# Optimization experiments

Measured on AMD Instinct MI355X. Metric: run time of the kernel, lower is better.

The kernel has to match this reference:

```python
import jax, jax.numpy as jnp
import numpy as np

N_NODES = 100000
N_EDGES = 1600000
N_GRAPHS = 1024
D_IN = 128
D_HID = 128
D_OUT = 2


def setup_inputs() -> dict:
    key = jax.random.key(0)
    ks = jax.random.split(key, 12)
    x = jax.random.normal(ks[0], (N_NODES, D_IN), dtype=jnp.float32)
    edge_index = jax.random.randint(ks[1], (2, N_EDGES), 0, N_NODES, dtype=jnp.int32)
    batch = jnp.sort(jax.random.randint(ks[2], (N_NODES,), 0, N_GRAPHS, dtype=jnp.int32))
    def lin(k, fan_in, fan_out):
        bound = 1.0 / np.sqrt(fan_in)
        kw, kb = jax.random.split(k)
        W = jax.random.uniform(kw, (fan_in, fan_out), minval=-bound, maxval=bound, dtype=jnp.float32)
        b = jax.random.uniform(kb, (fan_out,), minval=-bound, maxval=bound, dtype=jnp.float32)
        return W, b
    W1, b1 = lin(ks[3], D_IN, D_HID)
    W2, b2 = lin(ks[4], D_HID, D_HID)
    fc1_w, fc1_b = lin(ks[5], D_HID, D_HID)
    fc2_w, fc2_b = lin(ks[6], D_HID, D_OUT)
    return {"x": x, "edge_index": edge_index, "batch": batch,
            "W1": W1, "b1": b1, "W2": W2, "b2": b2,
            "fc1_w": fc1_w, "fc1_b": fc1_b, "fc2_w": fc2_w, "fc2_b": fc2_b}


def gcn_conv(x, W, b, src, dst, deg_inv_sqrt, n_nodes):
    # GCNConv: out = D^-1/2 (A + I) D^-1/2 (x W) + b, using edge list with self-loops
    h = x @ W  # [N, d_out]
    norm = deg_inv_sqrt[src] * deg_inv_sqrt[dst]  # [E+N]
    msg = h[src] * norm[:, None]  # gather + scale
    out = jnp.zeros((n_nodes, h.shape[1]), dtype=h.dtype).at[dst].add(msg)
    return out + b


def reference(x, edge_index, batch, W1, b1, W2, b2, fc1_w, fc1_b, fc2_w, fc2_b):
    n = x.shape[0]
    loops = jnp.arange(n, dtype=edge_index.dtype)
    src = jnp.concatenate([edge_index[0], loops])  # add self-loops (PyG default)
    dst = jnp.concatenate([edge_index[1], loops])
    deg = jnp.zeros((n,), dtype=x.dtype).at[dst].add(1.0)
    deg_inv_sqrt = jax.lax.rsqrt(deg)  # deg >= 1 due to self-loops

    h = jax.nn.relu(gcn_conv(x, W1, b1, src, dst, deg_inv_sqrt, n))
    # dropout p=0.5 is identity in eval mode
    h = jax.nn.relu(gcn_conv(h, W2, b2, src, dst, deg_inv_sqrt, n))

    # global_mean_pool over batch assignment
    sums = jax.ops.segment_sum(h, batch, num_segments=N_GRAPHS)
    cnts = jax.ops.segment_sum(jnp.ones((n,), dtype=h.dtype), batch, num_segments=N_GRAPHS)
    pooled = sums / jnp.maximum(cnts, 1.0)[:, None]  # [G, d]

    g = jax.nn.relu(pooled @ fc1_w + fc1_b)
    logits = g @ fc2_w + fc2_b
    return jax.nn.log_softmax(logits, axis=1)
```

## Files before the change

### kernel.cpp

```cpp
#include <hip/hip_runtime.h>
#include <hip/hip_fp16.h>
#include <math.h>


#define D_FEAT 128
#define BSHIFT 9
#define BNODES 512
#define CHUNK 4096
#define CAPB 16384

using half8   = __attribute__((ext_vector_type(8))) _Float16;
using half4   = __attribute__((ext_vector_type(4))) _Float16;
using floatx4 = __attribute__((ext_vector_type(4))) float;
using floatx2 = __attribute__((ext_vector_type(2))) float;

__global__ void __launch_bounds__(256) binA_kernel(const int* __restrict__ edges,
                                                   int* __restrict__ gcur,
                                                   int* __restrict__ binned, int E, int nb) {
    __shared__ int h[256];
    __shared__ int cur[256];
    __shared__ int base[256];
    int t = threadIdx.x;
    int c0 = blockIdx.x * CHUNK;
    int sv[CHUNK / 256], bv[CHUNK / 256];
    int i0 = c0 + t * (CHUNK / 256);
    if (i0 + (CHUNK / 256) <= E) {
#pragma unroll
        for (int k = 0; k < CHUNK / 256; k += 4) {
            int4 s4 = *(const int4*)&edges[i0 + k];
            int4 d4 = *(const int4*)&edges[E + i0 + k];
            bv[k + 0] = d4.x >> BSHIFT; sv[k + 0] = ((d4.x & (BNODES - 1)) << 17) | s4.x;
            bv[k + 1] = d4.y >> BSHIFT; sv[k + 1] = ((d4.y & (BNODES - 1)) << 17) | s4.y;
            bv[k + 2] = d4.z >> BSHIFT; sv[k + 2] = ((d4.z & (BNODES - 1)) << 17) | s4.z;
            bv[k + 3] = d4.w >> BSHIFT; sv[k + 3] = ((d4.w & (BNODES - 1)) << 17) | s4.w;
        }
    } else {
#pragma unroll
        for (int k = 0; k < CHUNK / 256; ++k) {
            int i = i0 + k;
            if (i < E) {
                int s = edges[i], d = edges[E + i];
                bv[k] = d >> BSHIFT;
                sv[k] = ((d & (BNODES - 1)) << 17) | s;
            } else bv[k] = -1;
        }
    }
    h[t] = 0;
    __syncthreads();
#pragma unroll
    for (int k = 0; k < CHUNK / 256; ++k)
        if (bv[k] >= 0) atomicAdd(&h[bv[k]], 1);
    __syncthreads();
    if (t < nb && h[t] > 0) base[t] = atomicAdd(&gcur[t], h[t]);
    cur[t] = 0;
    __syncthreads();
#pragma unroll
    for (int k = 0; k < CHUNK / 256; ++k)
        if (bv[k] >= 0) {
            int b = bv[k];
            int r = atomicAdd(&cur[b], 1);
            int pos = base[b] + r;
            if (pos < CAPB) binned[b * CAPB + pos] = sv[k];
        }
}

__global__ void __launch_bounds__(256) binB1_kernel(const int* __restrict__ binned,
                                                    const int* __restrict__ gcur,
                                                    float* __restrict__ dis,
                                                    int* __restrict__ rowptr,
                                                    int* __restrict__ gcursor,
                                                    int N, int E, int nb) {
    __shared__ int hist[BNODES];
    __shared__ int sdata[256];
    int t = threadIdx.x;
    int b = blockIdx.x;
    int node0 = b << BSHIFT;
    int cnt = gcur[b];
    int gval = (t < nb) ? gcur[t] : 0;
    sdata[t] = gval;
    __syncthreads();
    for (int d = 1; d < 256; d <<= 1) {
        int u = (t >= d) ? sdata[t - d] : 0;
        __syncthreads();
        sdata[t] += u;
        __syncthreads();
    }
    int e0 = sdata[b] - cnt;
    __syncthreads();
    const int* bin = binned + (size_t)b * CAPB;
    hist[t] = 0; hist[t + 256] = 0;
    __syncthreads();
    for (int i = t; i < cnt; i += 256) atomicAdd(&hist[bin[i] >> 17], 1);
    __syncthreads();
    int a0 = hist[2 * t], a1 = hist[2 * t + 1];
    int pair = a0 + a1;
    sdata[t] = pair;
    __syncthreads();
    for (int d = 1; d < 256; d <<= 1) {
        int u = (t >= d) ? sdata[t - d] : 0;
        __syncthreads();
        sdata[t] += u;
        __syncthreads();
    }
    int excl = sdata[t] - pair;
    int p0 = e0 + excl, p1 = e0 + excl + a0;
    gcursor[(b << BSHIFT) + 2 * t] = p0;
    gcursor[(b << BSHIFT) + 2 * t + 1] = p1;
    int n0 = node0 + 2 * t, n1 = node0 + 2 * t + 1;
    if (n0 < N) { rowptr[n0] = p0; dis[n0] = rsqrtf((float)a0 + 1.0f); }
    if (n1 < N) { rowptr[n1] = p1; dis[n1] = rsqrtf((float)a1 + 1.0f); }
    if (b == nb - 1 && t == 0) rowptr[N] = E;
}

__global__ void __launch_bounds__(256) binB2_kernel(const int* __restrict__ binned,
                                                    const int* __restrict__ gcur,
                                                    const int* __restrict__ gcursor,
                                                    int* __restrict__ csr, int nb) {
    __shared__ int cur[BNODES];
    int t = threadIdx.x;
    int b = blockIdx.x;
    int cnt = gcur[b];
    const int* bin = binned + (size_t)b * CAPB;
    cur[t] = gcursor[(b << BSHIFT) + t];
    cur[t + 256] = gcursor[(b << BSHIFT) + t + 256];
    __syncthreads();
    for (int i = t; i < cnt; i += 256) {
        int v = bin[i];
        int p = atomicAdd(&cur[v >> 17], 1);
        csr[p] = v & 0x1FFFF;
    }
}

__global__ void wprep_kernel(const float* __restrict__ W1, const float* __restrict__ W2,
                             _Float16* __restrict__ Wt1, _Float16* __restrict__ Wt2) {
    int i = blockIdx.x * blockDim.x + threadIdx.x;
    int n = i >> 7, k = i & 127;
    Wt1[i] = (_Float16)W1[k * 128 + n];
    Wt2[i] = (_Float16)W2[k * 128 + n];
}

template <bool HALF_IN>
__global__ void __launch_bounds__(256) gemm_mfma_kernel(const void* __restrict__ Xv,
                                                        const _Float16* __restrict__ WtG,
                                                        const float* __restrict__ dis,
                                                        unsigned char* __restrict__ Y8, int N) {
    __shared__ _Float16 wt[128][136];
    int t = threadIdx.x;
    int row0 = blockIdx.x * 64;

#pragma unroll
    for (int i = 0; i < 8; ++i) {
        int c = t + i * 256;
        int r = c >> 4, c8 = (c & 15) * 8;
        *(half8*)&wt[r][c8] = *(const half8*)&WtG[r * 128 + c8];
    }

    int wave = t >> 6, lane = t & 63;
    int m = lane & 15, quad = lane >> 4;
    int grow = row0 + wave * 16 + m;

    half8 a[4];
    if (grow < N) {
        if (HALF_IN) {
            const _Float16* Xp = (const _Float16*)Xv;
#pragma unroll
            for (int k = 0; k < 4; ++k)
                a[k] = *(const half8*)&Xp[(size_t)grow * 128 + k * 32 + quad * 8];
        } else {
            const float* Xp = (const float*)Xv;
#pragma unroll
            for (int k = 0; k < 4; ++k) {
                float4 v0 = *(const float4*)&Xp[(size_t)grow * 128 + k * 32 + quad * 8];
                float4 v1 = *(const float4*)&Xp[(size_t)grow * 128 + k * 32 + quad * 8 + 4];
                a[k] = (half8){(_Float16)v0.x, (_Float16)v0.y, (_Float16)v0.z, (_Float16)v0.w,
                               (_Float16)v1.x, (_Float16)v1.y, (_Float16)v1.z, (_Float16)v1.w};
            }
        }
    } else {
#pragma unroll
        for (int k = 0; k < 4; ++k) a[k] = (half8){};
    }
    __syncthreads();

    floatx4 acc[8];
#pragma unroll
    for (int nt = 0; nt < 8; ++nt) acc[nt] = (floatx4){0.f, 0.f, 0.f, 0.f};
#pragma unroll
    for (int nt = 0; nt < 8; ++nt) {
#pragma unroll
        for (int k = 0; k < 4; ++k) {
            half8 bfr = *(const half8*)&wt[nt * 16 + m][k * 32 + quad * 8];
            acc[nt] = __builtin_amdgcn_mfma_f32_16x16x32_f16(a[k], bfr, acc[nt], 0, 0, 0);
        }
    }
    int orow = row0 + wave * 16 + quad * 4;
#pragma unroll
    for (int r = 0; r < 4; ++r) {
        int row = orow + r;
        if (row < N) {
            float dr = dis[row];
#pragma unroll
            for (int nt = 0; nt < 8; ++nt) {
                float v = acc[nt][r] * dr;
                unsigned char q =
                    (unsigned char)(__builtin_amdgcn_cvt_pk_fp8_f32(v, v, 0, false) & 0xff);
                Y8[(size_t)row * 128 + nt * 16 + m] = q;
            }
        }
    }
}

__global__ void __launch_bounds__(256) agg_kernel(const unsigned char* __restrict__ H8,
                                                  const int* __restrict__ rowptr,
                                                  const int* __restrict__ csr,
                                                  const float* __restrict__ dis,
                                                  const float* __restrict__ bias,
                                                  _Float16* __restrict__ out, int N) {
    int v = (blockIdx.x * blockDim.x + threadIdx.x) >> 6;
    int lane = threadIdx.x & 63;
    if (v >= N) return;
    int half = lane >> 5, sl = lane & 31;
    int r0 = rowptr[v], r1 = rowptr[v + 1];
    float dv = dis[v];
    unsigned fo = (unsigned)(sl << 2);

    floatx2 a01, a23;
    {
        unsigned int u = *(const unsigned int*)(H8 + (((unsigned)v << 7) | fo));
        floatx2 lo = __builtin_amdgcn_cvt_pk_f32_fp8(u, false);
        floatx2 hi = __builtin_amdgcn_cvt_pk_f32_fp8(u, true);
        floatx2 hf = {0.5f, 0.5f};
        a01 = hf * lo;
        a23 = hf * hi;
    }
#define ACC(uu)                                                         \
        {                                                               \
            a01 += __builtin_amdgcn_cvt_pk_f32_fp8(uu, false);          \
            a23 += __builtin_amdgcn_cvt_pk_f32_fp8(uu, true);           \
        }
#define ACCW(uu, ww)                                                    \
        {                                                               \
            floatx2 w2 = {(ww), (ww)};                                  \
            a01 += w2 * __builtin_amdgcn_cvt_pk_f32_fp8(uu, false);     \
            a23 += w2 * __builtin_amdgcn_cvt_pk_f32_fp8(uu, true);      \
        }
    int e = r0 + half;
    for (; e + 14 < r1; e += 16) {
        int s0 = csr[e],      s1 = csr[e + 2],  s2 = csr[e + 4],  s3 = csr[e + 6];
        int s4 = csr[e + 8],  s5 = csr[e + 10], s6 = csr[e + 12], s7 = csr[e + 14];
        unsigned int u0 = *(const unsigned int*)(H8 + (((unsigned)s0 << 7) | fo));
        unsigned int u1 = *(const unsigned int*)(H8 + (((unsigned)s1 << 7) | fo));
        unsigned int u2 = *(const unsigned int*)(H8 + (((unsigned)s2 << 7) | fo));
        unsigned int u3 = *(const unsigned int*)(H8 + (((unsigned)s3 << 7) | fo));
        unsigned int u4 = *(const unsigned int*)(H8 + (((unsigned)s4 << 7) | fo));
        unsigned int u5 = *(const unsigned int*)(H8 + (((unsigned)s5 << 7) | fo));
        unsigned int u6 = *(const unsigned int*)(H8 + (((unsigned)s6 << 7) | fo));
        unsigned int u7 = *(const unsigned int*)(H8 + (((unsigned)s7 << 7) | fo));
        ACC(u0) ACC(u1) ACC(u2) ACC(u3) ACC(u4) ACC(u5) ACC(u6) ACC(u7)
    }
    if (e < r1) {
        int last = r1 - 1;
        int ss[8];
        unsigned int uu[8];
        float ww[8];
#pragma unroll
        for (int k = 0; k < 8; ++k) {
            int idx = e + 2 * k;
            ss[k] = csr[idx < last ? idx : last];
            ww[k] = (idx < r1) ? 1.f : 0.f;
        }
#pragma unroll
        for (int k = 0; k < 8; ++k)
            uu[k] = *(const unsigned int*)(H8 + (((unsigned)ss[k] << 7) | fo));
#pragma unroll
        for (int k = 0; k < 8; ++k) ACCW(uu[k], ww[k])
    }
#undef ACC
#undef ACCW
    a01[0] += __shfl_xor(a01[0], 32, 64);
    a01[1] += __shfl_xor(a01[1], 32, 64);
    a23[0] += __shfl_xor(a23[0], 32, 64);
    a23[1] += __shfl_xor(a23[1], 32, 64);
    if (half == 0) {
        float4 b = *(const float4*)&bias[sl * 4];
        half4 o = {(_Float16)fmaxf(dv * a01[0] + b.x, 0.f),
                   (_Float16)fmaxf(dv * a01[1] + b.y, 0.f),
                   (_Float16)fmaxf(dv * a23[0] + b.z, 0.f),
                   (_Float16)fmaxf(dv * a23[1] + b.w, 0.f)};
        *(half4*)&out[(size_t)v * 128 + sl * 4] = o;
    }
}

__device__ __forceinline__ int lower_bound_i(const int* a, int n, int key) {
    int lo = 0, hi = n;
    while (lo < hi) {
        int mid = (lo + hi) >> 1;
        if (a[mid] < key) lo = mid + 1;
        else hi = mid;
    }
    return lo;
}

__global__ void __launch_bounds__(512) pool_kernel(const _Float16* __restrict__ H,
                                                   const int* __restrict__ batch,
                                                   float* __restrict__ pooled, int N) {
    __shared__ int range[2];
    __shared__ float part[4][128];
    int g = blockIdx.x;
    int t = threadIdx.x;
    int j = t & 127, rg = t >> 7;
    if (t < 2) range[t] = lower_bound_i(batch, N, g + t);
    __syncthreads();
    int lo = range[0], hi = range[1];
    float s = 0.f;
    for (int v = lo + rg; v < hi; v += 4) s += (float)H[(size_t)v * 128 + j];
    part[rg][j] = s;
    __syncthreads();
    if (rg == 0) {
        float tot = part[0][j] + part[1][j] + part[2][j] + part[3][j];
        pooled[g * 128 + j] = tot / fmaxf((float)(hi - lo), 1.0f);
    }
}

__global__ void head_kernel(const float* __restrict__ pooled, const float* __restrict__ fc1w,
                            const float* __restrict__ fc1b, const float* __restrict__ fc2w,
                            const float* __restrict__ fc2b, float* __restrict__ out) {
    __shared__ float p[128];
    __shared__ float r0[128], r1[128];
    int g = blockIdx.x;
    int j = threadIdx.x;
    p[j] = pooled[g * 128 + j];
    __syncthreads();
    float acc = fc1b[j];
#pragma unroll 8
    for (int k = 0; k < 128; ++k) acc = fmaf(p[k], fc1w[k * 128 + j], acc);
    float gv = fmaxf(acc, 0.f);
    r0[j] = gv * fc2w[j * 2 + 0];
    r1[j] = gv * fc2w[j * 2 + 1];
    __syncthreads();
    for (int s = 64; s > 0; s >>= 1) {
        if (j < s) {
            r0[j] += r0[j + s];
            r1[j] += r1[j + s];
        }
        __syncthreads();
    }
    if (j == 0) {
        float l0 = r0[0] + fc2b[0];
        float l1 = r1[0] + fc2b[1];
        float m = fmaxf(l0, l1);
        float lse = m + logf(expf(l0 - m) + expf(l1 - m));
        out[g * 2 + 0] = l0 - lse;
        out[g * 2 + 1] = l1 - lse;
    }
}

extern "C" void kernel_launch(void* const* d_in, const int* in_sizes, int n_in,
                              void* d_out, int out_size, void* d_ws, size_t ws_size,
                              hipStream_t stream) {
    const float* x    = (const float*)d_in[0];
    const int* edges  = (const int*)d_in[1];
    const int* batch  = (const int*)d_in[2];
    const float* W1   = (const float*)d_in[3];
    const float* b1   = (const float*)d_in[4];
    const float* W2   = (const float*)d_in[5];
    const float* b2   = (const float*)d_in[6];
    const float* fc1w = (const float*)d_in[7];
    const float* fc1b = (const float*)d_in[8];
    const float* fc2w = (const float*)d_in[9];
    const float* fc2b = (const float*)d_in[10];
    float* out = (float*)d_out;

    int N = in_sizes[2];
    int E = in_sizes[1] / 2;
    int G = out_size / 2;
    int nb = (N + BNODES - 1) / BNODES;
    int nA = (E + CHUNK - 1) / CHUNK;

    char* ws = (char*)d_ws;
    size_t off = 0;
    auto alloc = [&](size_t bytes) -> char* {
        char* ptr = ws + off;
        off += (bytes + 255) & ~(size_t)255;
        return ptr;
    };
    int* gcur          = (int*)alloc((size_t)nb * 4);
    int* binned        = (int*)alloc((size_t)nb * CAPB * 4);
    int* rowptr        = (int*)alloc((size_t)(N + 1) * 4);
    float* dis         = (float*)alloc((size_t)N * 4);
    int* gcursor       = (int*)alloc((size_t)nb * BNODES * 4);
    int* csr           = (int*)alloc((size_t)E * 4);
    _Float16* Wt1      = (_Float16*)alloc(128 * 128 * 2);
    _Float16* Wt2      = (_Float16*)alloc(128 * 128 * 2);
    unsigned char* buf8 = (unsigned char*)alloc((size_t)N * D_FEAT);
    _Float16* bufH     = (_Float16*)alloc((size_t)N * D_FEAT * 2);
    float* pooled      = (float*)alloc((size_t)G * D_FEAT * 4);

    hipMemsetAsync(gcur, 0, (size_t)nb * 4, stream);

    binA_kernel<<<nA, 256, 0, stream>>>(edges, gcur, binned, E, nb);
    binB1_kernel<<<nb, 256, 0, stream>>>(binned, gcur, dis, rowptr, gcursor, N, E, nb);
    binB2_kernel<<<nb, 256, 0, stream>>>(binned, gcur, gcursor, csr, nb);
    wprep_kernel<<<64, 256, 0, stream>>>(W1, W2, Wt1, Wt2);

    int gAgg = (N * 64 + 255) / 256;
    int gGemm = (N + 63) / 64;
    gemm_mfma_kernel<false><<<gGemm, 256, 0, stream>>>((const void*)x, Wt1, dis, buf8, N);
    agg_kernel<<<gAgg, 256, 0, stream>>>(buf8, rowptr, csr, dis, b1, bufH, N);
    gemm_mfma_kernel<true><<<gGemm, 256, 0, stream>>>((const void*)bufH, Wt2, dis, buf8, N);
    agg_kernel<<<gAgg, 256, 0, stream>>>(buf8, rowptr, csr, dis, b2, bufH, N);
    pool_kernel<<<G, 512, 0, stream>>>(bufH, batch, pooled, N);
    head_kernel<<<G, 128, 0, stream>>>(pooled, fc1w, fc1b, fc2w, fc2b, out);
}
```

Measured before the change: 282.0 us.

## Pad CSR rows to multiples of 16 with zero-row sentinel, fuse bin and pool/head kernels

Each node's adjacency list is padded to a multiple of 16 entries, and the padding points at an extra all-zero row in the fp8 feature buffer. This lets the aggregation loop drop its masked tail path. The two binning passes are merged into one kernel that caches bin values in LDS and writes per-block CSR regions with begin/end arrays, which removes the global prefix scan. Pooling and the MLP head are fused into one kernel. In exchange, padding adds extra gathers of the zero row, and the fixed per-block capacities (PCAP, CAP) could overflow on denser graphs.

```diff
diff --git a/kernel.cpp b/kernel.cpp
--- a/kernel.cpp
+++ b/kernel.cpp
@@ -8,6 +8,8 @@
 #define BNODES 512
 #define CHUNK 4096
 #define CAPB 16384
+#define PCAP 16384
+#define CAP 10240
 
 using half8   = __attribute__((ext_vector_type(8))) _Float16;
 using half4   = __attribute__((ext_vector_type(4))) _Float16;
@@ -64,20 +66,35 @@
         }
 }
 
-__global__ void __launch_bounds__(256) binB1_kernel(const int* __restrict__ binned,
-                                                    const int* __restrict__ gcur,
-                                                    float* __restrict__ dis,
-                                                    int* __restrict__ rowptr,
-                                                    int* __restrict__ gcursor,
-                                                    int N, int E, int nb) {
+__global__ void __launch_bounds__(256) binB_kernel(const int* __restrict__ binned,
+                                                   const int* __restrict__ gcur,
+                                                   float* __restrict__ dis,
+                                                   int* __restrict__ rowbeg,
+                                                   int* __restrict__ rowend,
+                                                   int* __restrict__ csr,
+                                                   int N, int nb) {
     __shared__ int hist[BNODES];
+    __shared__ int cur[BNODES];
+    __shared__ int pend[BNODES];
     __shared__ int sdata[256];
+    __shared__ int vals[CAP];
     int t = threadIdx.x;
     int b = blockIdx.x;
     int node0 = b << BSHIFT;
     int cnt = gcur[b];
-    int gval = (t < nb) ? gcur[t] : 0;
-    sdata[t] = gval;
+    const int* bin = binned + (size_t)b * CAPB;
+    hist[t] = 0; hist[t + 256] = 0;
+    __syncthreads();
+    for (int i = t; i < cnt; i += 256) {
+        int v = bin[i];
+        if (i < CAP) vals[i] = v;
+        atomicAdd(&hist[v >> 17], 1);
+    }
+    __syncthreads();
+    int a0 = hist[2 * t], a1 = hist[2 * t + 1];
+    int p0sz = (a0 + 15) & ~15, p1sz = (a1 + 15) & ~15;
+    int pair = p0sz + p1sz;
+    sdata[t] = pair;
     __syncthreads();
     for (int d = 1; d < 256; d <<= 1) {
         int u = (t >= d) ? sdata[t - d] : 0;
@@ -85,58 +102,42 @@
         sdata[t] += u;
         __syncthreads();
     }
-    int e0 = sdata[b] - cnt;
-    __syncthreads();
-    const int* bin = binned + (size_t)b * CAPB;
-    hist[t] = 0; hist[t + 256] = 0;
-    __syncthreads();
-    for (int i = t; i < cnt; i += 256) atomicAdd(&hist[bin[i] >> 17], 1);
-    __syncthreads();
-    int a0 = hist[2 * t], a1 = hist[2 * t + 1];
-    int pair = a0 + a1;
-    sdata[t] = pair;
-    __syncthreads();
-    for (int d = 1; d < 256; d <<= 1) {
-        int u = (t >= d) ? sdata[t - d] : 0;
-        __syncthreads();
-        sdata[t] += u;
-        __syncthreads();
-    }
     int excl = sdata[t] - pair;
-    int p0 = e0 + excl, p1 = e0 + excl + a0;
-    gcursor[(b << BSHIFT) + 2 * t] = p0;
-    gcursor[(b << BSHIFT) + 2 * t + 1] = p1;
+    int q0 = b * PCAP + excl, q1 = q0 + p0sz;
+    cur[2 * t] = q0;
+    cur[2 * t + 1] = q1;
+    pend[2 * t] = q1;
+    pend[2 * t + 1] = q1 + p1sz;
     int n0 = node0 + 2 * t, n1 = node0 + 2 * t + 1;
-    if (n0 < N) { rowptr[n0] = p0; dis[n0] = rsqrtf((float)a0 + 1.0f); }
-    if (n1 < N) { rowptr[n1] = p1; dis[n1] = rsqrtf((float)a1 + 1.0f); }
-    if (b == nb - 1 && t == 0) rowptr[N] = E;
-}
-
-__global__ void __launch_bounds__(256) binB2_kernel(const int* __restrict__ binned,
-                                                    const int* __restrict__ gcur,
-                                                    const int* __restrict__ gcursor,
-                                                    int* __restrict__ csr, int nb) {
-    __shared__ int cur[BNODES];
-    int t = threadIdx.x;
-    int b = blockIdx.x;
-    int cnt = gcur[b];
-    const int* bin = binned + (size_t)b * CAPB;
-    cur[t] = gcursor[(b << BSHIFT) + t];
-    cur[t + 256] = gcursor[(b << BSHIFT) + t + 256];
+    if (n0 < N) {
+        rowbeg[n0] = q0; rowend[n0] = q1;
+        dis[n0] = rsqrtf((float)a0 + 1.0f);
+    }
+    if (n1 < N) {
+        rowbeg[n1] = q1; rowend[n1] = q1 + p1sz;
+        dis[n1] = rsqrtf((float)a1 + 1.0f);
+    }
     __syncthreads();
     for (int i = t; i < cnt; i += 256) {
-        int v = bin[i];
+        int v = (i < CAP) ? vals[i] : bin[i];
         int p = atomicAdd(&cur[v >> 17], 1);
         csr[p] = v & 0x1FFFF;
     }
+    __syncthreads();
+    for (int i = t; i < BNODES; i += 256) {
+        int e = pend[i];
+        for (int p = cur[i]; p < e; ++p) csr[p] = N;
+    }
 }
 
 __global__ void wprep_kernel(const float* __restrict__ W1, const float* __restrict__ W2,
-                             _Float16* __restrict__ Wt1, _Float16* __restrict__ Wt2) {
+                             _Float16* __restrict__ Wt1, _Float16* __restrict__ Wt2,
+                             unsigned int* __restrict__ zrow) {
     int i = blockIdx.x * blockDim.x + threadIdx.x;
     int n = i >> 7, k = i & 127;
     Wt1[i] = (_Float16)W1[k * 128 + n];
     Wt2[i] = (_Float16)W2[k * 128 + n];
+    if (i < 32) zrow[i] = 0u;
 }
 
 template <bool HALF_IN>
@@ -211,7 +212,8 @@
 }
 
 __global__ void __launch_bounds__(256) agg_kernel(const unsigned char* __restrict__ H8,
-                                                  const int* __restrict__ rowptr,
+                                                  const int* __restrict__ rowbeg,
+                                                  const int* __restrict__ rowend,
                                                   const int* __restrict__ csr,
                                                   const float* __restrict__ dis,
                                                   const float* __restrict__ bias,
@@ -220,7 +222,7 @@
     int lane = threadIdx.x & 63;
     if (v >= N) return;
     int half = lane >> 5, sl = lane & 31;
-    int r0 = rowptr[v], r1 = rowptr[v + 1];
+    int r0 = rowbeg[v], r1 = rowend[v];
     float dv = dis[v];
     unsigned fo = (unsigned)(sl << 2);
 
@@ -238,14 +240,7 @@
             a01 += __builtin_amdgcn_cvt_pk_f32_fp8(uu, false);          \
             a23 += __builtin_amdgcn_cvt_pk_f32_fp8(uu, true);           \
         }
-#define ACCW(uu, ww)                                                    \
-        {                                                               \
-            floatx2 w2 = {(ww), (ww)};                                  \
-            a01 += w2 * __builtin_amdgcn_cvt_pk_f32_fp8(uu, false);     \
-            a23 += w2 * __builtin_amdgcn_cvt_pk_f32_fp8(uu, true);      \
-        }
-    int e = r0 + half;
-    for (; e + 14 < r1; e += 16) {
+    for (int e = r0 + half; e + 14 < r1; e += 16) {
         int s0 = csr[e],      s1 = csr[e + 2],  s2 = csr[e + 4],  s3 = csr[e + 6];
         int s4 = csr[e + 8],  s5 = csr[e + 10], s6 = csr[e + 12], s7 = csr[e + 14];
         unsigned int u0 = *(const unsigned int*)(H8 + (((unsigned)s0 << 7) | fo));
@@ -258,25 +253,7 @@
         unsigned int u7 = *(const unsigned int*)(H8 + (((unsigned)s7 << 7) | fo));
         ACC(u0) ACC(u1) ACC(u2) ACC(u3) ACC(u4) ACC(u5) ACC(u6) ACC(u7)
     }
-    if (e < r1) {
-        int last = r1 - 1;
-        int ss[8];
-        unsigned int uu[8];
-        float ww[8];
-#pragma unroll
-        for (int k = 0; k < 8; ++k) {
-            int idx = e + 2 * k;
-            ss[k] = csr[idx < last ? idx : last];
-            ww[k] = (idx < r1) ? 1.f : 0.f;
-        }
-#pragma unroll
-        for (int k = 0; k < 8; ++k)
-            uu[k] = *(const unsigned int*)(H8 + (((unsigned)ss[k] << 7) | fo));
-#pragma unroll
-        for (int k = 0; k < 8; ++k) ACCW(uu[k], ww[k])
-    }
 #undef ACC
-#undef ACCW
     a01[0] += __shfl_xor(a01[0], 32, 64);
     a01[1] += __shfl_xor(a01[1], 32, 64);
     a23[0] += __shfl_xor(a23[0], 32, 64);
@@ -301,11 +278,17 @@
     return lo;
 }
 
-__global__ void __launch_bounds__(512) pool_kernel(const _Float16* __restrict__ H,
-                                                   const int* __restrict__ batch,
-                                                   float* __restrict__ pooled, int N) {
+__global__ void __launch_bounds__(512) poolhead_kernel(const _Float16* __restrict__ H,
+                                                       const int* __restrict__ batch,
+                                                       const float* __restrict__ fc1w,
+                                                       const float* __restrict__ fc1b,
+                                                       const float* __restrict__ fc2w,
+                                                       const float* __restrict__ fc2b,
+                                                       float* __restrict__ out, int N) {
     __shared__ int range[2];
     __shared__ float part[4][128];
+    __shared__ float p[128];
+    __shared__ float r0s[128], r1s[128];
     int g = blockIdx.x;
     int t = threadIdx.x;
     int j = t & 127, rg = t >> 7;
@@ -318,36 +301,28 @@
     __syncthreads();
     if (rg == 0) {
         float tot = part[0][j] + part[1][j] + part[2][j] + part[3][j];
-        pooled[g * 128 + j] = tot / fmaxf((float)(hi - lo), 1.0f);
-    }
-}
-
-__global__ void head_kernel(const float* __restrict__ pooled, const float* __restrict__ fc1w,
-                            const float* __restrict__ fc1b, const float* __restrict__ fc2w,
-                            const float* __restrict__ fc2b, float* __restrict__ out) {
-    __shared__ float p[128];
-    __shared__ float r0[128], r1[128];
-    int g = blockIdx.x;
-    int j = threadIdx.x;
-    p[j] = pooled[g * 128 + j];
-    __syncthreads();
-    float acc = fc1b[j];
+        p[j] = tot / fmaxf((float)(hi - lo), 1.0f);
+    }
+    __syncthreads();
+    if (t < 128) {
+        float acc = fc1b[t];
 #pragma unroll 8
-    for (int k = 0; k < 128; ++k) acc = fmaf(p[k], fc1w[k * 128 + j], acc);
-    float gv = fmaxf(acc, 0.f);
-    r0[j] = gv * fc2w[j * 2 + 0];
-    r1[j] = gv * fc2w[j * 2 + 1];
-    __syncthreads();
-    for (int s = 64; s > 0; s >>= 1) {
-        if (j < s) {
-            r0[j] += r0[j + s];
-            r1[j] += r1[j + s];
+        for (int k = 0; k < 128; ++k) acc = fmaf(p[k], fc1w[k * 128 + t], acc);
+        float gv = fmaxf(acc, 0.f);
+        r0s[t] = gv * fc2w[t * 2 + 0];
+        r1s[t] = gv * fc2w[t * 2 + 1];
+    }
+    __syncthreads();
+    for (int st = 64; st > 0; st >>= 1) {
+        if (t < st) {
+            r0s[t] += r0s[t + st];
+            r1s[t] += r1s[t + st];
         }
         __syncthreads();
     }
-    if (j == 0) {
-        float l0 = r0[0] + fc2b[0];
-        float l1 = r1[0] + fc2b[1];
+    if (t == 0) {
+        float l0 = r0s[0] + fc2b[0];
+        float l1 = r1s[0] + fc2b[1];
         float m = fmaxf(l0, l1);
         float lse = m + logf(expf(l0 - m) + expf(l1 - m));
         out[g * 2 + 0] = l0 - lse;
@@ -386,29 +361,27 @@
     };
     int* gcur          = (int*)alloc((size_t)nb * 4);
     int* binned        = (int*)alloc((size_t)nb * CAPB * 4);
-    int* rowptr        = (int*)alloc((size_t)(N + 1) * 4);
+    int* rowbeg        = (int*)alloc((size_t)N * 4);
+    int* rowend        = (int*)alloc((size_t)N * 4);
     float* dis         = (float*)alloc((size_t)N * 4);
-    int* gcursor       = (int*)alloc((size_t)nb * BNODES * 4);
-    int* csr           = (int*)alloc((size_t)E * 4);
+    int* csr           = (int*)alloc((size_t)nb * PCAP * 4);
     _Float16* Wt1      = (_Float16*)alloc(128 * 128 * 2);
     _Float16* Wt2      = (_Float16*)alloc(128 * 128 * 2);
-    unsigned char* buf8 = (unsigned char*)alloc((size_t)N * D_FEAT);
+    unsigned char* buf8 = (unsigned char*)alloc((size_t)(N + 1) * D_FEAT);
     _Float16* bufH     = (_Float16*)alloc((size_t)N * D_FEAT * 2);
-    float* pooled      = (float*)alloc((size_t)G * D_FEAT * 4);
 
     hipMemsetAsync(gcur, 0, (size_t)nb * 4, stream);
 
     binA_kernel<<<nA, 256, 0, stream>>>(edges, gcur, binned, E, nb);
-    binB1_kernel<<<nb, 256, 0, stream>>>(binned, gcur, dis, rowptr, gcursor, N, E, nb);
-    binB2_kernel<<<nb, 256, 0, stream>>>(binned, gcur, gcursor, csr, nb);
-    wprep_kernel<<<64, 256, 0, stream>>>(W1, W2, Wt1, Wt2);
+    binB_kernel<<<nb, 256, 0, stream>>>(binned, gcur, dis, rowbeg, rowend, csr, N, nb);
+    wprep_kernel<<<64, 256, 0, stream>>>(W1, W2, Wt1, Wt2,
+                                         (unsigned int*)(buf8 + (size_t)N * D_FEAT));
 
     int gAgg = (N * 64 + 255) / 256;
     int gGemm = (N + 63) / 64;
     gemm_mfma_kernel<false><<<gGemm, 256, 0, stream>>>((const void*)x, Wt1, dis, buf8, N);
-    agg_kernel<<<gAgg, 256, 0, stream>>>(buf8, rowptr, csr, dis, b1, bufH, N);
+    agg_kernel<<<gAgg, 256, 0, stream>>>(buf8, rowbeg, rowend, csr, dis, b1, bufH, N);
     gemm_mfma_kernel<true><<<gGemm, 256, 0, stream>>>((const void*)bufH, Wt2, dis, buf8, N);
-    agg_kernel<<<gAgg, 256, 0, stream>>>(buf8, rowptr, csr, dis, b2, bufH, N);
-    pool_kernel<<<G, 512, 0, stream>>>(bufH, batch, pooled, N);
-    head_kernel<<<G, 128, 0, stream>>>(pooled, fc1w, fc1b, fc2w, fc2b, out);
-}
+    agg_kernel<<<gAgg, 256, 0, stream>>>(buf8, rowbeg, rowend, csr, dis, b2, bufH, N);
+    poolhead_kernel<<<G, 512, 0, stream>>>(bufH, batch, fc1w, fc1b, fc2w, fc2b, out, N);
+}
```

Measured after the change: 266.5 us. -5.5%, faster.
